# Optimization experiments

Measured on AMD Instinct MI355X. Metric: run time of the kernel, lower is better.

## Reference

```python
import jax, jax.numpy as jnp
import numpy as np

OUT = 7          # out_size
SCALE = 0.25     # spatial_scale
SAMPLE = 2       # sample_num (samples per bin edge)
NORI = 8         # nOrientation
TWO_PI = 2.0 * np.pi


def setup_inputs() -> dict:
    key = jax.random.key(0)
    k1, k2, k3, k4, k5 = jax.random.split(key, 5)
    N, C, H, W = 2, 256, 128, 128
    R = 4096
    features = jax.random.normal(k1, (N, C, H, W), dtype=jnp.float32)
    # rois: (batch_idx, cx, cy, w, h, theta) in image coords (image ~512x512)
    bidx = jax.random.randint(k2, (R, 1), 0, N).astype(jnp.float32)
    cxy = jax.random.uniform(k3, (R, 2), minval=32.0, maxval=480.0, dtype=jnp.float32)
    wh = jax.random.uniform(k4, (R, 2), minval=16.0, maxval=256.0, dtype=jnp.float32)
    theta = jax.random.uniform(k5, (R, 1), minval=0.0, maxval=TWO_PI, dtype=jnp.float32)
    rois = jnp.concatenate([bidx, cxy, wh, theta], axis=1)
    return {"features": features, "rois": rois}


def riroi_align(features, rois):
    """Rotation-invariant RoIAlign (ReDet RiRoIAlign) forward.

    features: [N, C, H, W] with C = c_per * NORI, channel layout c*NORI + o.
    rois:     [R, 6] = (batch_idx, cx, cy, w, h, theta).
    returns:  [R, C, OUT, OUT]
    """
    N, C, H, W = features.shape
    c_per = C // NORI
    g = SAMPLE

    def one_roi(roi):
        b = roi[0].astype(jnp.int32)
        cx = roi[1] * SCALE
        cy = roi[2] * SCALE
        rw = jnp.maximum(roi[3] * SCALE, 1.0)
        rh = jnp.maximum(roi[4] * SCALE, 1.0)
        theta = roi[5]
        bin_w = rw / OUT
        bin_h = rh / OUT
        idx = jnp.arange(OUT, dtype=jnp.float32)
        off = (jnp.arange(g, dtype=jnp.float32) + 0.5) / g
        # local (un-rotated) sample coords, roi-centered; P = OUT*g points per axis
        yy = (-rh / 2 + idx[:, None] * bin_h + off[None, :] * bin_h).reshape(-1)
        xx = (-rw / 2 + idx[:, None] * bin_w + off[None, :] * bin_w).reshape(-1)
        c_t, s_t = jnp.cos(theta), jnp.sin(theta)
        x = xx[None, :] * c_t + yy[:, None] * s_t + cx   # [P, P]
        y = yy[:, None] * c_t - xx[None, :] * s_t + cy   # [P, P]

        # bilinear interpolation with RoIAlign border conventions
        valid = (y > -1.0) & (y < H) & (x > -1.0) & (x < W)
        xc = jnp.clip(x, 0.0, None)
        yc = jnp.clip(y, 0.0, None)
        x0 = jnp.floor(xc).astype(jnp.int32)
        y0 = jnp.floor(yc).astype(jnp.int32)
        hx = x0 >= W - 1
        hy = y0 >= H - 1
        x0 = jnp.where(hx, W - 1, x0)
        x1 = jnp.where(hx, W - 1, x0 + 1)
        y0 = jnp.where(hy, H - 1, y0)
        y1 = jnp.where(hy, H - 1, y0 + 1)
        xc = jnp.where(hx, x0.astype(jnp.float32), xc)
        yc = jnp.where(hy, y0.astype(jnp.float32), yc)
        lx = xc - x0
        ly = yc - y0
        wx0 = 1.0 - lx
        wy0 = 1.0 - ly

        def gat(yi, xi):
            return features[b, :, yi, xi]  # [P, P, C]

        val = ((wy0 * wx0)[..., None] * gat(y0, x0)
               + (wy0 * lx)[..., None] * gat(y0, x1)
               + (ly * wx0)[..., None] * gat(y1, x0)
               + (ly * lx)[..., None] * gat(y1, x1))
        val = jnp.where(valid[..., None], val, 0.0)       # [P, P, C]
        val = jnp.moveaxis(val, -1, 0)                    # [C, P, P]
        # average the g x g samples within each output bin
        val = val.reshape(C, OUT, g, OUT, g).mean(axis=(2, 4))  # [C, OUT, OUT]

        # orientation-channel circular rotation with linear interpolation
        ind_f = theta * NORI / TWO_PI
        ind0 = jnp.floor(ind_f)
        l = ind_f - ind0
        ind = ind0.astype(jnp.int32) % NORI
        o = jnp.arange(NORI)
        src = (o - ind) % NORI
        src_p = (src + 1) % NORI
        v = val.reshape(c_per, NORI, OUT, OUT)
        out = (1.0 - l) * v[:, src] + l * v[:, src_p]
        return out.reshape(C, OUT, OUT)

    return jax.vmap(one_roi)(rois)  # [R, C, OUT, OUT]


def reference(features, rois):
    return riroi_align(features, rois)
```

## Files before the change

### kernel.cpp

```cpp
#include <hip/hip_runtime.h>

typedef _Float16 half_t;
typedef int   v2i __attribute__((ext_vector_type(2)));
typedef int   v4i __attribute__((ext_vector_type(4)));
typedef float v4f __attribute__((ext_vector_type(4)));

#define OUTS 7
#define NORI 8
#define NCH  256
#define FH   128
#define FW   128
#define HW   (FH * FW)
#define NSAMP (2 * OUTS * 2 * OUTS)
#define NBIN  (OUTS * OUTS)
#define WBINS 7
#define NBKT  512

__global__ __launch_bounds__(256) void transpose_nchw_nhwc_h(
    const float* __restrict__ in, half_t* __restrict__ out) {
  __shared__ float tile[64][65];
  const int b  = blockIdx.z;
  const int p0 = blockIdx.x * 64;
  const int c0 = blockIdx.y * 64;
  const int tx = threadIdx.x & 63;
  const int ty = threadIdx.x >> 6;

  const float* src = in + ((size_t)b * NCH + c0) * HW + p0;
#pragma unroll
  for (int i = 0; i < 16; ++i) {
    int c = ty + i * 4;
    tile[c][tx] = src[(size_t)c * HW + tx];
  }
  __syncthreads();
  half_t* dst = out + ((size_t)b * HW + p0) * NCH + c0;
#pragma unroll
  for (int i = 0; i < 16; ++i) {
    int p = ty + i * 4;
    dst[(size_t)p * NCH + tx] = (half_t)tile[tx][p];
  }
}

__global__ __launch_bounds__(256) void key_hist_kernel(
    const float* __restrict__ rois, int R, int* __restrict__ hist,
    int* __restrict__ keys) {
  const int i = blockIdx.x * 256 + threadIdx.x;
  if (i >= R) return;
  const float* roi = rois + (size_t)i * 6;
  const int b  = ((int)roi[0]) & 1;
  int mx = (((int)roi[1]) >> 5) & 15;
  int my = (((int)roi[2]) >> 5) & 15;
  mx = (mx | (mx << 2)) & 0x33; mx = (mx | (mx << 1)) & 0x55;
  my = (my | (my << 2)) & 0x33; my = (my | (my << 1)) & 0x55;
  const int key = (b << 8) | mx | (my << 1);
  keys[i] = key;
  atomicAdd(&hist[key], 1);
}

__global__ __launch_bounds__(NBKT) void scan_kernel(
    const int* __restrict__ hist, int* __restrict__ cursor) {
  __shared__ int s[NBKT];
  const int t = threadIdx.x;
  const int v = hist[t];
  s[t] = v;
  __syncthreads();
  for (int off = 1; off < NBKT; off <<= 1) {
    const int add = (t >= off) ? s[t - off] : 0;
    __syncthreads();
    s[t] += add;
    __syncthreads();
  }
  cursor[t] = s[t] - v;
}

__global__ __launch_bounds__(256) void scatter_kernel(
    const int* __restrict__ keys, int R, int* __restrict__ cursor,
    int* __restrict__ order) {
  const int i = blockIdx.x * 256 + threadIdx.x;
  if (i >= R) return;
  const int pos = atomicAdd(&cursor[keys[i]], 1);
  order[pos] = i;
}

#define FMALO(accv, wv, pk) \
  asm("v_fma_mix_f32 %0, %1, %2, %0 op_sel_hi:[0,1,0]" \
      : "+v"(accv) : "v"(wv), "v"(pk))
#define FMAHI(accv, wv, pk) \
  asm("v_fma_mix_f32 %0, %1, %2, %0 op_sel:[0,1,0] op_sel_hi:[0,1,0]" \
      : "+v"(accv) : "v"(wv), "v"(pk))

template <bool SORTED>
__global__ __launch_bounds__(512) void riroi_main(
    const half_t* __restrict__ feat, const float* __restrict__ rois,
    const int* __restrict__ order, float* __restrict__ out) {
  __shared__ v4i s_geom[NSAMP * 2];
  __shared__ alignas(16) float s_tr[64 * NBIN];

  const int t = threadIdx.x;
  const int w = t >> 6;
  const int l = t & 63;
  const int b0 = w * 6;
  const int gbase = w * 24;

  int r;
  if (SORTED) {
    const int bid = blockIdx.x, nwg = gridDim.x;
    const int virt = ((nwg & 7) == 0) ? ((bid & 7) * (nwg >> 3) + (bid >> 3))
                                      : bid;
    r = order[virt];
  } else {
    r = blockIdx.x;
  }

  const float* roi = rois + (size_t)r * 6;
  const float theta = roi[5];

  if (t < NSAMP) {
    const int bin = t >> 2;
    const int sub = t & 3;
    const int by = bin / OUTS, bx = bin - by * OUTS;
    const int py = by * 2 + (sub >> 1);
    const int px = bx * 2 + (sub & 1);

    const int   b  = (int)roi[0];
    const float cx = roi[1] * 0.25f;
    const float cy = roi[2] * 0.25f;
    const float rw = fmaxf(roi[3] * 0.25f, 1.0f);
    const float rh = fmaxf(roi[4] * 0.25f, 1.0f);
    const float bin_w = rw * (1.0f / OUTS);
    const float bin_h = rh * (1.0f / OUTS);
    const float ct = cosf(theta), st = sinf(theta);
    const float hbw = 0.5f * bin_w, hbh = 0.5f * bin_h;
    const float xoff = 0.25f * bin_w - 0.5f * rw;
    const float yoff = 0.25f * bin_h - 0.5f * rh;

    const float yy = (float)py * hbh + yoff;
    const float xx = (float)px * hbw + xoff;
    const float x = xx * ct + yy * st + cx;
    const float y = yy * ct - xx * st + cy;

    v4i oo = {0, 0, 0, 0};
    v4f ww = {0.f, 0.f, 0.f, 0.f};
    if (x > -1.0f && x < (float)FW && y > -1.0f && y < (float)FH) {
      float xc = fmaxf(x, 0.f);
      float yc = fmaxf(y, 0.f);
      int x0 = (int)xc;
      int y0 = (int)yc;
      int x1, y1;
      float lx, ly;
      if (x0 >= FW - 1) { x0 = FW - 1; x1 = FW - 1; lx = 0.f; }
      else              { x1 = x0 + 1; lx = xc - (float)x0; }
      if (y0 >= FH - 1) { y0 = FH - 1; y1 = FH - 1; ly = 0.f; }
      else              { y1 = y0 + 1; ly = yc - (float)y0; }
      const float wx0 = 1.f - lx, wy0 = 1.f - ly;
      ww.x = 0.25f * wy0 * wx0; ww.y = 0.25f * wy0 * lx;
      ww.z = 0.25f * ly  * wx0; ww.w = 0.25f * ly  * lx;
      const int base = b * HW;
      oo.x = (base + y0 * FW + x0) << 9; oo.y = (base + y0 * FW + x1) << 9;
      oo.z = (base + y1 * FW + x0) << 9; oo.w = (base + y1 * FW + x1) << 9;
    }
    s_geom[2 * t]     = oo;
    s_geom[2 * t + 1] = *(v4i*)&ww;
  }
  __syncthreads();

  const float indf = theta * (8.0f / 6.2831853071795862f);
  const float ind0 = floorf(indf);
  const float lmix = indf - ind0;
  const int   ind  = ((int)ind0) & 7;
  const int   m    = (8 - ind) & 7;

  const char* fb = (const char*)feat;
  const unsigned lane_off = (unsigned)(l << 3);

  float acc[WBINS][4];
#pragma unroll
  for (int i = 0; i < WBINS; ++i)
#pragma unroll
    for (int j = 0; j < 4; ++j) acc[i][j] = 0.f;

#define DECLSET(S) \
  v4i og##S; v4f wg##S; v2i va##S, vb##S, vc##S, vd##S;
  DECLSET(P) DECLSET(Q)
#undef DECLSET

#define GSTAGE(S, bt) { \
  const int gi = gbase + (bt); \
  og##S = s_geom[2 * gi]; wg##S = *(const v4f*)&s_geom[2 * gi + 1]; }

#define VSTAGE(S) { \
  va##S = *(const v2i*)(fb + ((unsigned)og##S.x + lane_off)); \
  vb##S = *(const v2i*)(fb + ((unsigned)og##S.y + lane_off)); \
  vc##S = *(const v2i*)(fb + ((unsigned)og##S.z + lane_off)); \
  vd##S = *(const v2i*)(fb + ((unsigned)og##S.w + lane_off)); }

#define FTAP(wv, pk, p) { \
  FMALO(acc[p][0], wv, pk.x); FMAHI(acc[p][1], wv, pk.x); \
  FMALO(acc[p][2], wv, pk.y); FMAHI(acc[p][3], wv, pk.y); }

#define FSTAGE(S, p) \
  FTAP(wg##S.x, va##S, p) FTAP(wg##S.y, vb##S, p) \
  FTAP(wg##S.z, vc##S, p) FTAP(wg##S.w, vd##S, p)

#define ITER(bt, CUR, NXT) { \
  if ((bt) + 1 < 28) { GSTAGE(NXT, (bt) + 1); VSTAGE(NXT); } \
  __builtin_amdgcn_s_setprio(1); \
  FSTAGE(CUR, (bt) / 4); \
  __builtin_amdgcn_s_setprio(0); }

  GSTAGE(P, 0) VSTAGE(P)
  ITER(0,  P, Q) ITER(1,  Q, P) ITER(2,  P, Q) ITER(3,  Q, P)
  ITER(4,  P, Q) ITER(5,  Q, P) ITER(6,  P, Q) ITER(7,  Q, P)
  ITER(8,  P, Q) ITER(9,  Q, P) ITER(10, P, Q) ITER(11, Q, P)
  ITER(12, P, Q) ITER(13, Q, P) ITER(14, P, Q) ITER(15, Q, P)
  ITER(16, P, Q) ITER(17, Q, P) ITER(18, P, Q) ITER(19, Q, P)
  ITER(20, P, Q) ITER(21, Q, P) ITER(22, P, Q) ITER(23, Q, P)
  ITER(24, P, Q) ITER(25, Q, P) ITER(26, P, Q) ITER(27, Q, P)

#undef ITER
#undef FSTAGE
#undef FTAP
#undef VSTAGE
#undef GSTAGE

#define MIX_BODY(M)                                                        \
  {                                                                        \
    _Pragma("unroll")                                                      \
    for (int bb = 0; bb < WBINS; ++bb) {                                   \
      float B[8];                                                          \
      B[0] = acc[bb][0]; B[1] = acc[bb][1];                                \
      B[2] = acc[bb][2]; B[3] = acc[bb][3];                                \
      B[4] = __shfl_xor(acc[bb][0], 1, 64);                                \
      B[5] = __shfl_xor(acc[bb][1], 1, 64);                                \
      B[6] = __shfl_xor(acc[bb][2], 1, 64);                                \
      B[7] = __shfl_xor(acc[bb][3], 1, 64);                                \
      float tt[4];                                                         \
      _Pragma("unroll")                                                    \
      for (int j = 0; j < 4; ++j) {                                        \
        const float a0 = B[((M) + j) & 7];                                 \
        const float a1 = B[((M) + j + 1) & 7];                             \
        tt[j] = a0 + lmix * (a1 - a0);                                     \
      }                                                                    \
      acc[bb][0] = tt[0]; acc[bb][1] = tt[1];                              \
      acc[bb][2] = tt[2]; acc[bb][3] = tt[3];                              \
    }                                                                      \
  }
  switch (m) {
    case 0: MIX_BODY(0) break;
    case 1: MIX_BODY(1) break;
    case 2: MIX_BODY(2) break;
    case 3: MIX_BODY(3) break;
    case 4: MIX_BODY(4) break;
    case 5: MIX_BODY(5) break;
    case 6: MIX_BODY(6) break;
    case 7: MIX_BODY(7) break;
  }
#undef MIX_BODY

#pragma unroll
  for (int g = 0; g < 4; ++g) {
    if ((l >> 4) == g) {
      const int cl = (l & 15) * 4;
#pragma unroll
      for (int bb = 0; bb < WBINS; ++bb) {
        const int bin = b0 + bb;
#pragma unroll
        for (int j = 0; j < 4; ++j)
          s_tr[(cl + j) * NBIN + bin] = acc[bb][j];
      }
    }
    __syncthreads();
    const v4f* s4 = (const v4f*)s_tr;
    v4f* d4 = (v4f*)(out + (size_t)r * (NCH * NBIN) + g * (64 * NBIN));
    for (int i = t; i < 64 * NBIN / 4; i += 512)
      __builtin_nontemporal_store(s4[i], d4 + i);
    __syncthreads();
  }
}

__global__ __launch_bounds__(256) void riroi_cf(
    const float* __restrict__ feat, const float* __restrict__ rois,
    float* __restrict__ out) {
  const int r = blockIdx.x;
  const int c = threadIdx.x;
  const float* roi = rois + (size_t)r * 6;
  const int   b     = (int)roi[0];
  const float cx    = roi[1] * 0.25f;
  const float cy    = roi[2] * 0.25f;
  const float rw    = fmaxf(roi[3] * 0.25f, 1.0f);
  const float rh    = fmaxf(roi[4] * 0.25f, 1.0f);
  const float theta = roi[5];
  const float bin_w = rw * (1.0f / OUTS), bin_h = rh * (1.0f / OUTS);
  const float ct = cosf(theta), st = sinf(theta);
  const float hbw = 0.5f * bin_w, hbh = 0.5f * bin_h;
  const float xoff = 0.25f * bin_w - 0.5f * rw;
  const float yoff = 0.25f * bin_h - 0.5f * rh;
  const float* fb = feat + ((size_t)b * NCH + c) * HW;
  float acc[NBIN];
#pragma unroll
  for (int i = 0; i < NBIN; ++i) acc[i] = 0.f;
  for (int py = 0; py < 2 * OUTS; ++py) {
    const float yy = (float)py * hbh + yoff;
    for (int px = 0; px < 2 * OUTS; ++px) {
      const float xx = (float)px * hbw + xoff;
      const float x = xx * ct + yy * st + cx;
      const float y = yy * ct - xx * st + cy;
      if (x > -1.0f && x < (float)FW && y > -1.0f && y < (float)FH) {
        float xc = fmaxf(x, 0.f), yc = fmaxf(y, 0.f);
        int x0 = (int)xc, y0 = (int)yc, x1, y1;
        float lx, ly;
        if (x0 >= FW - 1) { x0 = FW - 1; x1 = FW - 1; lx = 0.f; }
        else              { x1 = x0 + 1; lx = xc - (float)x0; }
        if (y0 >= FH - 1) { y0 = FH - 1; y1 = FH - 1; ly = 0.f; }
        else              { y1 = y0 + 1; ly = yc - (float)y0; }
        const float wx0 = 1.f - lx, wy0 = 1.f - ly;
        acc[(py >> 1) * OUTS + (px >> 1)] +=
            (wy0 * wx0) * fb[y0 * FW + x0] + (wy0 * lx) * fb[y0 * FW + x1]
          + (ly * wx0) * fb[y1 * FW + x0] + (ly * lx) * fb[y1 * FW + x1];
      }
    }
  }
#pragma unroll
  for (int i = 0; i < NBIN; ++i) acc[i] *= 0.25f;
  const float indf = (theta * 8.0f) / 6.2831853071795862f;
  const float ind0 = floorf(indf);
  const float l    = indf - ind0;
  const int   ind  = ((int)ind0) % NORI;
  const int   o    = c & 7;
  const int   lane = c & 63;
  const int srcLane  = (lane & 56) | ((o - ind + 8) & 7);
  const int srcLane2 = (lane & 56) | ((o - ind + 9) & 7);
  float* op = out + ((size_t)r * NCH + c) * NBIN;
#pragma unroll
  for (int i = 0; i < NBIN; ++i) {
    const float v  = acc[i];
    const float vs = __shfl(v, srcLane, 64);
    const float vp = __shfl(v, srcLane2, 64);
    op[i] = (1.f - l) * vs + l * vp;
  }
}

extern "C" void kernel_launch(void* const* d_in, const int* in_sizes, int n_in,
                              void* d_out, int out_size, void* d_ws, size_t ws_size,
                              hipStream_t stream) {
  const float* feat = (const float*)d_in[0];
  const float* rois = (const float*)d_in[1];
  float* out = (float*)d_out;
  const int R = in_sizes[1] / 6;
  const int N = in_sizes[0] / (NCH * HW);

  const size_t sort_bytes = ((size_t)(2 * NBKT + 2 * R) * 4 + 255) & ~(size_t)255;
  const size_t feat_bytes = (size_t)N * HW * NCH * sizeof(half_t);
  const int rb = (R + 255) / 256;

  if (ws_size >= sort_bytes + feat_bytes) {
    int*    hist   = (int*)d_ws;
    int*    cursor = hist + NBKT;
    int*    keys   = cursor + NBKT;
    int*    order  = keys + R;
    half_t* ft = (half_t*)((char*)d_ws + sort_bytes);

    hipMemsetAsync(hist, 0, NBKT * sizeof(int), stream);
    key_hist_kernel<<<rb, 256, 0, stream>>>(rois, R, hist, keys);
    scan_kernel<<<1, NBKT, 0, stream>>>(hist, cursor);
    scatter_kernel<<<rb, 256, 0, stream>>>(keys, R, cursor, order);

    dim3 tg(HW / 64, NCH / 64, N);
    transpose_nchw_nhwc_h<<<tg, 256, 0, stream>>>(feat, ft);
    riroi_main<true><<<R, 512, 0, stream>>>(ft, rois, order, out);
  } else if (ws_size >= feat_bytes) {
    half_t* ft = (half_t*)d_ws;
    dim3 tg(HW / 64, NCH / 64, N);
    transpose_nchw_nhwc_h<<<tg, 256, 0, stream>>>(feat, ft);
    riroi_main<false><<<R, 512, 0, stream>>>(ft, rois, nullptr, out);
  } else {
    riroi_cf<<<R, 256, 0, stream>>>(feat, rois, out);
  }
}
```

Before: 138.3 us.

## Fetch bilinear x-neighbours with one 16-byte row load per lane half

The kernel now exploits the fact that the x0 and x0+1 pixels are adjacent in the NHWC half-precision layout. It issues two 16-byte loads per sample, one per row, instead of four 8-byte tap loads. Lanes 0-31 accumulate the left pixel and lanes 32-63 the right pixel, each holding 8 channels, i.e. a full orientation group. The halves are then combined with an xor-32 shuffle, so the orientation mix no longer needs a neighbour shuffle. The right-border case is handled by shifting the base column and moving the weight. In exchange, the per-lane accumulator count doubles, which raises register pressure and adds cross-half shuffles.

```diff
diff --git a/kernel.cpp b/kernel.cpp
--- a/kernel.cpp
+++ b/kernel.cpp
@@ -92,12 +92,15 @@
 __global__ __launch_bounds__(512) void riroi_main(
     const half_t* __restrict__ feat, const float* __restrict__ rois,
     const int* __restrict__ order, float* __restrict__ out) {
-  __shared__ v4i s_geom[NSAMP * 2];
+  __shared__ v2i s_go[NSAMP];
+  __shared__ v4f s_gw[NSAMP];
   __shared__ alignas(16) float s_tr[64 * NBIN];
 
   const int t = threadIdx.x;
   const int w = t >> 6;
   const int l = t & 63;
+  const int s = l & 31;
+  const int h = l >> 5;
   const int b0 = w * 6;
   const int gbase = w * 24;
 
@@ -138,28 +141,29 @@
     const float x = xx * ct + yy * st + cx;
     const float y = yy * ct - xx * st + cy;
 
-    v4i oo = {0, 0, 0, 0};
+    v2i oo = {0, 0};
     v4f ww = {0.f, 0.f, 0.f, 0.f};
     if (x > -1.0f && x < (float)FW && y > -1.0f && y < (float)FH) {
       float xc = fmaxf(x, 0.f);
       float yc = fmaxf(y, 0.f);
       int x0 = (int)xc;
       int y0 = (int)yc;
-      int x1, y1;
+      int y1;
       float lx, ly;
-      if (x0 >= FW - 1) { x0 = FW - 1; x1 = FW - 1; lx = 0.f; }
-      else              { x1 = x0 + 1; lx = xc - (float)x0; }
+      int ox; float wxl, wxh;
+      if (x0 >= FW - 1) { ox = FW - 2; wxl = 0.f; wxh = 1.f; }
+      else              { ox = x0; lx = xc - (float)x0; wxl = 1.f - lx; wxh = lx; }
       if (y0 >= FH - 1) { y0 = FH - 1; y1 = FH - 1; ly = 0.f; }
       else              { y1 = y0 + 1; ly = yc - (float)y0; }
-      const float wx0 = 1.f - lx, wy0 = 1.f - ly;
-      ww.x = 0.25f * wy0 * wx0; ww.y = 0.25f * wy0 * lx;
-      ww.z = 0.25f * ly  * wx0; ww.w = 0.25f * ly  * lx;
+      const float wy0 = 1.f - ly, wy1 = ly;
+      ww.x = 0.25f * wy0 * wxl; ww.y = 0.25f * wy0 * wxh;
+      ww.z = 0.25f * wy1 * wxl; ww.w = 0.25f * wy1 * wxh;
       const int base = b * HW;
-      oo.x = (base + y0 * FW + x0) << 9; oo.y = (base + y0 * FW + x1) << 9;
-      oo.z = (base + y1 * FW + x0) << 9; oo.w = (base + y1 * FW + x1) << 9;
+      oo.x = (base + y0 * FW + ox) << 9;
+      oo.y = (base + y1 * FW + ox) << 9;
     }
-    s_geom[2 * t]     = oo;
-    s_geom[2 * t + 1] = *(v4i*)&ww;
+    s_go[t] = oo;
+    s_gw[t] = ww;
   }
   __syncthreads();
 
@@ -170,36 +174,37 @@
   const int   m    = (8 - ind) & 7;
 
   const char* fb = (const char*)feat;
-  const unsigned lane_off = (unsigned)(l << 3);
-
-  float acc[WBINS][4];
+  const unsigned lane16 = (unsigned)(l << 4);
+
+  float acc[WBINS][8];
 #pragma unroll
   for (int i = 0; i < WBINS; ++i)
 #pragma unroll
-    for (int j = 0; j < 4; ++j) acc[i][j] = 0.f;
+    for (int j = 0; j < 8; ++j) acc[i][j] = 0.f;
 
 #define DECLSET(S) \
-  v4i og##S; v4f wg##S; v2i va##S, vb##S, vc##S, vd##S;
+  v2i og##S; float wA##S, wB##S; v4i va##S, vb##S;
   DECLSET(P) DECLSET(Q)
 #undef DECLSET
 
 #define GSTAGE(S, bt) { \
   const int gi = gbase + (bt); \
-  og##S = s_geom[2 * gi]; wg##S = *(const v4f*)&s_geom[2 * gi + 1]; }
+  og##S = s_go[gi]; \
+  const v4f wg = s_gw[gi]; \
+  wA##S = h ? wg.y : wg.x; \
+  wB##S = h ? wg.w : wg.z; }
 
 #define VSTAGE(S) { \
-  va##S = *(const v2i*)(fb + ((unsigned)og##S.x + lane_off)); \
-  vb##S = *(const v2i*)(fb + ((unsigned)og##S.y + lane_off)); \
-  vc##S = *(const v2i*)(fb + ((unsigned)og##S.z + lane_off)); \
-  vd##S = *(const v2i*)(fb + ((unsigned)og##S.w + lane_off)); }
-
-#define FTAP(wv, pk, p) { \
+  va##S = *(const v4i*)(fb + ((unsigned)og##S.x + lane16)); \
+  vb##S = *(const v4i*)(fb + ((unsigned)og##S.y + lane16)); }
+
+#define FROW(wv, pk, p) { \
   FMALO(acc[p][0], wv, pk.x); FMAHI(acc[p][1], wv, pk.x); \
-  FMALO(acc[p][2], wv, pk.y); FMAHI(acc[p][3], wv, pk.y); }
-
-#define FSTAGE(S, p) \
-  FTAP(wg##S.x, va##S, p) FTAP(wg##S.y, vb##S, p) \
-  FTAP(wg##S.z, vc##S, p) FTAP(wg##S.w, vd##S, p)
+  FMALO(acc[p][2], wv, pk.y); FMAHI(acc[p][3], wv, pk.y); \
+  FMALO(acc[p][4], wv, pk.z); FMAHI(acc[p][5], wv, pk.z); \
+  FMALO(acc[p][6], wv, pk.w); FMAHI(acc[p][7], wv, pk.w); }
+
+#define FSTAGE(S, p) FROW(wA##S, va##S, p) FROW(wB##S, vb##S, p)
 
 #define ITER(bt, CUR, NXT) { \
   if ((bt) + 1 < 28) { GSTAGE(NXT, (bt) + 1); VSTAGE(NXT); } \
@@ -218,30 +223,29 @@
 
 #undef ITER
 #undef FSTAGE
-#undef FTAP
+#undef FROW
 #undef VSTAGE
 #undef GSTAGE
+
+#pragma unroll
+  for (int bb = 0; bb < WBINS; ++bb)
+#pragma unroll
+    for (int j = 0; j < 8; ++j)
+      acc[bb][j] += __shfl_xor(acc[bb][j], 32, 64);
 
 #define MIX_BODY(M)                                                        \
   {                                                                        \
     _Pragma("unroll")                                                      \
     for (int bb = 0; bb < WBINS; ++bb) {                                   \
-      float B[8];                                                          \
-      B[0] = acc[bb][0]; B[1] = acc[bb][1];                                \
-      B[2] = acc[bb][2]; B[3] = acc[bb][3];                                \
-      B[4] = __shfl_xor(acc[bb][0], 1, 64);                                \
-      B[5] = __shfl_xor(acc[bb][1], 1, 64);                                \
-      B[6] = __shfl_xor(acc[bb][2], 1, 64);                                \
-      B[7] = __shfl_xor(acc[bb][3], 1, 64);                                \
-      float tt[4];                                                         \
+      float tt[8];                                                         \
       _Pragma("unroll")                                                    \
-      for (int j = 0; j < 4; ++j) {                                        \
-        const float a0 = B[((M) + j) & 7];                                 \
-        const float a1 = B[((M) + j + 1) & 7];                             \
+      for (int j = 0; j < 8; ++j) {                                        \
+        const float a0 = acc[bb][((M) + j) & 7];                           \
+        const float a1 = acc[bb][((M) + j + 1) & 7];                       \
         tt[j] = a0 + lmix * (a1 - a0);                                     \
       }                                                                    \
-      acc[bb][0] = tt[0]; acc[bb][1] = tt[1];                              \
-      acc[bb][2] = tt[2]; acc[bb][3] = tt[3];                              \
+      _Pragma("unroll")                                                    \
+      for (int j = 0; j < 8; ++j) acc[bb][j] = tt[j];                      \
     }                                                                      \
   }
   switch (m) {
@@ -258,14 +262,14 @@
 
 #pragma unroll
   for (int g = 0; g < 4; ++g) {
-    if ((l >> 4) == g) {
-      const int cl = (l & 15) * 4;
+    if ((s >> 3) == g) {
+      const int clb = (s & 7) * 8 + h * 4;
 #pragma unroll
       for (int bb = 0; bb < WBINS; ++bb) {
         const int bin = b0 + bb;
 #pragma unroll
-        for (int j = 0; j < 4; ++j)
-          s_tr[(cl + j) * NBIN + bin] = acc[bb][j];
+        for (int jj = 0; jj < 4; ++jj)
+          s_tr[(clb + jj) * NBIN + bin] = acc[bb][h * 4 + jj];
       }
     }
     __syncthreads();
```

Measured after the change: 287.1 us. 108% more time.
